# Kernel optimization log

Hardware: AMD Instinct MI355X
Metric: run time of the kernel (lower is better)

The kernel has to match this reference:

```python
import jax, jax.numpy as jnp
import numpy as np

B, S, D_IN, H, D_K = 4, 2048, 512, 8, 64
EPS = 1e-5

def _layer_norm(x, gamma, beta):
    mu = jnp.mean(x, axis=-1, keepdims=True)
    var = jnp.var(x, axis=-1, keepdims=True)
    return (x - mu) * jax.lax.rsqrt(var + EPS) * gamma + beta

def setup_inputs() -> dict:
    key = jax.random.key(0)
    ks = jax.random.split(key, 8)
    d_model = H * D_K
    scale = 1.0 / np.sqrt(D_IN)
    inp = {
        "q": jax.random.normal(ks[0], (B, S, D_IN), jnp.float32),
        "k": jax.random.normal(ks[1], (B, S, D_IN), jnp.float32),
        "v": jax.random.normal(ks[2], (B, S, D_IN), jnp.float32),
        "mask": jnp.ones((B, 1, S, S), jnp.float32),
        "Wq": jax.random.normal(ks[3], (D_IN, d_model), jnp.float32) * scale,
        "bq": jnp.zeros((d_model,), jnp.float32),
        "Wk": jax.random.normal(ks[4], (D_IN, d_model), jnp.float32) * scale,
        "bk": jnp.zeros((d_model,), jnp.float32),
        "Wv": jax.random.normal(ks[5], (D_IN, d_model), jnp.float32) * scale,
        "bv": jnp.zeros((d_model,), jnp.float32),
        "Wo": jax.random.normal(ks[6], (d_model, D_IN), jnp.float32) * (1.0 / np.sqrt(d_model)),
        "bo": jnp.zeros((D_IN,), jnp.float32),
        "gamma": jnp.ones((D_IN,), jnp.float32),
        "beta": jnp.zeros((D_IN,), jnp.float32),
    }
    return inp

def reference(q, k, v, mask, Wq, bq, Wk, bk, Wv, bv, Wo, bo, gamma, beta):
    b, sq, _ = q.shape
    # QKV projections, split heads: [B,S,H*Dk] -> [B,H,S,Dk]
    qh = (q @ Wq + bq).reshape(b, sq, H, D_K).transpose(0, 2, 1, 3)
    kh = (k @ Wk + bk).reshape(b, -1, H, D_K).transpose(0, 2, 1, 3)
    vh = (v @ Wv + bv).reshape(b, -1, H, D_K).transpose(0, 2, 1, 3)
    # scores with multiplicative mask + threshold (non-standard, per source)
    scores = jnp.einsum('bhqd,bhkd->bhqk', qh, kh) / np.sqrt(D_K)
    scores = scores * mask  # mask broadcasts over heads (repeat in torch)
    scores = jnp.where(scores > 0, scores, jnp.float32(-10000.0))
    attn = jax.nn.softmax(scores, axis=-1)
    out = jnp.einsum('bhqk,bhkd->bhqd', attn, vh)
    out = out.transpose(0, 2, 1, 3).reshape(b, sq, H * D_K)
    out = out @ Wo + bo
    return _layer_norm(q + out, gamma, beta)
```

## Files before the change

kernel.cpp:

```cpp
#include <hip/hip_runtime.h>
#include <stdint.h>

typedef __attribute__((ext_vector_type(8))) short s16x8;
typedef __attribute__((ext_vector_type(4))) float f32x4;

__device__ __forceinline__ unsigned short f2bf(float f){
  union { float f; unsigned u; } v; v.f = f;
  return (unsigned short)((v.u + 0x7FFFu + ((v.u>>16)&1u))>>16);
}
__device__ __forceinline__ float bf2f(unsigned short u){
  union { unsigned u; float f; } c; c.u = ((unsigned)u)<<16; return c.f;
}
#if __has_builtin(__builtin_amdgcn_cvt_pk_bf16_f32)
__device__ __forceinline__ unsigned pkbf(float a, float b){
  typedef __attribute__((ext_vector_type(2))) __bf16 bf16x2;
  union { bf16x2 v; unsigned u; } c;
  c.v = __builtin_amdgcn_cvt_pk_bf16_f32(a, b);
  return c.u;
}
#else
__device__ __forceinline__ unsigned pkbf(float a, float b){
  return (unsigned)f2bf(a) | ((unsigned)f2bf(b)<<16);
}
#endif

__device__ __forceinline__ void g2l16(const void* g, void* l){
  auto* lp = reinterpret_cast<__attribute__((address_space(3))) unsigned int*>(
      reinterpret_cast<uintptr_t>(l));
  auto* gp = reinterpret_cast<const __attribute__((address_space(1))) unsigned int*>(
      reinterpret_cast<uintptr_t>(g));
  __builtin_amdgcn_global_load_lds(gp, lp, 16, 0, 0);
}

__global__ __launch_bounds__(256) void cvt_all(
    const float* __restrict__ mask, const float* __restrict__ q,
    const float* __restrict__ k,    const float* __restrict__ v,
    unsigned short* __restrict__ mo, unsigned short* __restrict__ qo,
    unsigned short* __restrict__ ko, unsigned short* __restrict__ vo)
{
  const int z = blockIdx.z;
  const float* src = (z==0)?mask:(z==1)?q:(z==2)?k:v;
  unsigned short* dst = (z==0)?mo:(z==1)?qo:(z==2)?ko:vo;
  const int n = (z==0) ? 4*2048*2048 : 8192*512;
  const int i8 = (blockIdx.x*256 + threadIdx.x)*8;
  if (i8 < n){
    const float4 a = *(const float4*)&src[i8];
    const float4 b = *(const float4*)&src[i8+4];
    uint4 o;
    o.x = pkbf(a.x,a.y); o.y = pkbf(a.z,a.w);
    o.z = pkbf(b.x,b.y); o.w = pkbf(b.z,b.w);
    *(uint4*)&dst[i8] = o;
  }
}

__global__ __launch_bounds__(256) void convert_wT(
    const float* __restrict__ W0, const float* __restrict__ W1,
    const float* __restrict__ W2, const float* __restrict__ W3,
    unsigned short* __restrict__ T0, unsigned short* __restrict__ T1,
    unsigned short* __restrict__ T2, unsigned short* __restrict__ T3)
{
  __shared__ float Ts[64][65];
  const int z = blockIdx.z;
  const float* W = (z==0)?W0:(z==1)?W1:(z==2)?W2:W3;
  unsigned short* Wt = (z==0)?T0:(z==1)?T1:(z==2)?T2:T3;
  const int t = threadIdx.x;
  const int k0 = blockIdx.x*64, n0 = blockIdx.y*64;
  {
    const int r = t>>4, c = (t&15)*4;
#pragma unroll
    for (int rr=0; rr<4; ++rr){
      const float4 w4 = *(const float4*)&W[(size_t)(k0 + r + rr*16)*512 + n0 + c];
      Ts[r+rr*16][c]   = w4.x; Ts[r+rr*16][c+1] = w4.y;
      Ts[r+rr*16][c+2] = w4.z; Ts[r+rr*16][c+3] = w4.w;
    }
  }
  __syncthreads();
  const int n = t>>2, kc = (t&3)*16;
  unsigned o[8];
#pragma unroll
  for (int i=0;i<16;i+=2) o[i>>1] = pkbf(Ts[kc+i][n], Ts[kc+i+1][n]);
  *(uint4*)&Wt[(size_t)(n0+n)*512 + k0 + kc]     = *(uint4*)&o[0];
  *(uint4*)&Wt[(size_t)(n0+n)*512 + k0 + kc + 8] = *(uint4*)&o[4];
}

template<int EPI>
__global__ __launch_bounds__(256) void gemm_m97(
    const unsigned short* __restrict__ A0, const unsigned short* __restrict__ A1,
    const unsigned short* __restrict__ A2,
    const unsigned short* __restrict__ W0, const unsigned short* __restrict__ W1,
    const unsigned short* __restrict__ W2,
    const float* __restrict__ b0, const float* __restrict__ b1, const float* __restrict__ b2,
    unsigned short* __restrict__ Oq, unsigned short* __restrict__ Ok,
    unsigned short* __restrict__ Ov, unsigned short* __restrict__ Oflat)
{
  __shared__ unsigned short As[128*64];
  __shared__ unsigned short Bs[128*64];
  const int t = threadIdx.x;
  const int lane = t & 63;
  const int w = t >> 6;
  const int l16 = lane & 15;
  const int quad = lane >> 4;
  const int wm = w & 1, wn = w >> 1;
  const int bm = blockIdx.x, bn = blockIdx.y;
  const int z = (EPI==0) ? (int)blockIdx.z : 0;
  const unsigned short* A  = (z==0)?A0:(z==1)?A1:A2;
  const unsigned short* Wt = (z==0)?W0:(z==1)?W1:W2;
  const float* bias        = (z==0)?b0:(z==1)?b1:b2;

  const int Lr = lane >> 3;
  const int gc = (lane & 7) ^ Lr;

  f32x4 acc[4][4];
#pragma unroll
  for(int i=0;i<4;i++)
#pragma unroll
    for(int j=0;j<4;j++) acc[i][j] = (f32x4){0.f,0.f,0.f,0.f};

  for (int kt=0; kt<8; ++kt){
    const int k0 = kt*64;
#pragma unroll
    for (int j=0;j<4;++j){
      const int rb = w*32 + j*8;
      g2l16(&A [(size_t)(bm*128 + rb + Lr)*512 + k0 + gc*8], &As[rb*64]);
      g2l16(&Wt[(size_t)(bn*128 + rb + Lr)*512 + k0 + gc*8], &Bs[rb*64]);
    }
    __syncthreads();
#pragma unroll
    for (int kk=0;kk<2;++kk){
      s16x8 af[4], bfr[4];
#pragma unroll
      for (int mt=0;mt<4;++mt){
        const int row = wm*64 + mt*16 + l16;
        af[mt] = *(const s16x8*)&As[row*64 + (((kk*4+quad) ^ (row&7))*8)];
      }
#pragma unroll
      for (int nt=0;nt<4;++nt){
        const int row = wn*64 + nt*16 + l16;
        bfr[nt] = *(const s16x8*)&Bs[row*64 + (((kk*4+quad) ^ (row&7))*8)];
      }
#pragma unroll
      for (int mt=0;mt<4;++mt)
#pragma unroll
        for (int nt=0;nt<4;++nt)
          acc[mt][nt] = __builtin_amdgcn_mfma_f32_16x16x32_bf16(af[mt], bfr[nt], acc[mt][nt], 0,0,0);
    }
    __syncthreads();
  }

#pragma unroll
  for (int mt=0;mt<4;++mt){
    const int gm = bm*128 + wm*64 + mt*16 + quad*4;
    const int b_ = gm>>11, s = gm & 2047;
#pragma unroll
    for (int nt=0;nt<4;++nt){
      const int gn = bn*128 + wn*64 + nt*16 + l16;
      const float bv = bias[gn];
      if (EPI==1){
#pragma unroll
        for (int r=0;r<4;++r)
          Oflat[(size_t)(gm+r)*512 + gn] = f2bf(acc[mt][nt][r] + bv);
      } else if (z==2){
        const int hh = gn>>6, dk = gn&63;
        uint2 uu;
        uu.x = pkbf(acc[mt][nt][0]+bv, acc[mt][nt][1]+bv);
        uu.y = pkbf(acc[mt][nt][2]+bv, acc[mt][nt][3]+bv);
        *(uint2*)&Ov[(((size_t)b_*8 + hh)*64 + dk)*2048 + s] = uu;
      } else {
        const int hh = gn>>6, dk = gn&63;
        unsigned short* Out = (z==0)?Oq:Ok;
        const float scl = (z==0)?0.125f:1.0f;
#pragma unroll
        for (int r=0;r<4;++r)
          Out[(((size_t)b_*8 + hh)*2048 + (s+r))*64 + dk] = f2bf((acc[mt][nt][r]+bv)*scl);
      }
    }
  }
}

__global__ __launch_bounds__(512,4) void attn_kernel(
    const unsigned short* __restrict__ Qp, const unsigned short* __restrict__ Kp,
    const unsigned short* __restrict__ Vt, const unsigned short* __restrict__ maskb,
    unsigned short* __restrict__ Ap)
{
  __shared__ unsigned short Ks[2][64*64];
  __shared__ unsigned short Vs[2][64*64];
  const int t = threadIdx.x;
  const int lane = t & 63;
  const int w = t >> 6;
  const int l16 = lane & 15;
  const int quad = lane >> 4;
  const int h = blockIdx.x, qt = blockIdx.y, b = blockIdx.z;
  const int q0 = qt*128;
  const unsigned short* Qb = Qp + (((size_t)b*8 + h)*2048 + q0)*64;
  const unsigned short* Kb = Kp + ((size_t)b*8 + h)*2048*64;
  const unsigned short* Vb = Vt + ((size_t)b*8 + h)*64*2048;
  const unsigned short* mb = maskb + (size_t)b*2048*2048;

  s16x8 qf[2];
#pragma unroll
  for (int kk=0;kk<2;++kk)
    qf[kk] = *(const s16x8*)&Qb[(size_t)(w*16 + l16)*64 + kk*32 + quad*8];

  const int Lr = lane >> 3;
  const int gc = (lane & 7) ^ Lr;
  const int srow = w*8 + Lr;

  g2l16(&Kb[(size_t)srow*64   + gc*8], &Ks[0][w*8*64]);
  g2l16(&Vb[(size_t)srow*2048 + gc*8], &Vs[0][w*8*64]);

  f32x4 o_acc[4];
#pragma unroll
  for(int nt=0;nt<4;++nt) o_acc[nt]=(f32x4){0.f,0.f,0.f,0.f};
  float l_run = 0.f;

  union U8 { unsigned u[4]; s16x8 v; };
  const int gq = q0 + w*16 + l16;

  for (int kt=0; kt<32; ++kt){
    const int cur = kt&1;
    const int kbase = kt*64;
    __syncthreads();

    uint2 mr[4];
    {
      const unsigned short* mrow = mb + (size_t)gq*2048 + kbase + quad*4;
#pragma unroll
      for (int nt=0;nt<4;++nt) mr[nt] = *(const uint2*)&mrow[nt*16];
    }
    if (kt<31){
      const int kb2 = (kt+1)*64;
      g2l16(&Kb[(size_t)(kb2+srow)*64 + gc*8],   &Ks[cur^1][w*8*64]);
      g2l16(&Vb[(size_t)srow*2048 + kb2 + gc*8], &Vs[cur^1][w*8*64]);
    }

    f32x4 sc[4];
#pragma unroll
    for(int nt=0;nt<4;++nt) sc[nt]=(f32x4){0.f,0.f,0.f,0.f};
#pragma unroll
    for (int nt=0;nt<4;++nt){
      const int row = nt*16 + l16;
      const int rx = row & 7;
      const s16x8 kf0 = *(const s16x8*)&Ks[cur][row*64 + ((quad ^ rx)*8)];
      const s16x8 kf1 = *(const s16x8*)&Ks[cur][row*64 + (((4+quad) ^ rx)*8)];
      sc[nt] = __builtin_amdgcn_mfma_f32_16x16x32_bf16(kf0, qf[0], sc[nt],0,0,0);
      sc[nt] = __builtin_amdgcn_mfma_f32_16x16x32_bf16(kf1, qf[1], sc[nt],0,0,0);
    }
    unsigned pk[8];
    float rs = 0.f;
#pragma unroll
    for (int nt=0;nt<4;++nt){
      const float m0 = bf2f((unsigned short)(mr[nt].x & 0xffffu));
      const float m1 = bf2f((unsigned short)(mr[nt].x >> 16));
      const float m2 = bf2f((unsigned short)(mr[nt].y & 0xffffu));
      const float m3 = bf2f((unsigned short)(mr[nt].y >> 16));
      float x0 = sc[nt][0]*m0, x1 = sc[nt][1]*m1, x2 = sc[nt][2]*m2, x3 = sc[nt][3]*m3;
      x0 = (x0>0.f)?x0:-10000.f; x1 = (x1>0.f)?x1:-10000.f;
      x2 = (x2>0.f)?x2:-10000.f; x3 = (x3>0.f)?x3:-10000.f;
      const float e0 = __expf(x0), e1 = __expf(x1), e2 = __expf(x2), e3 = __expf(x3);
      rs += (e0+e1)+(e2+e3);
      pk[nt*2]   = pkbf(e0, e1);
      pk[nt*2+1] = pkbf(e2, e3);
    }
    rs += __shfl_xor(rs, 16);
    rs += __shfl_xor(rs, 32);
    l_run += rs;
    U8 pu[2];
#pragma unroll
    for (int kk=0;kk<2;++kk)
#pragma unroll
      for (int c=0;c<4;++c){
        const int srcLane = (((quad&1)*2 + (c>>1))<<4) | l16;
        const int vA = __shfl((int)pk[kk*4 + (c&1)],     srcLane);
        const int vB = __shfl((int)pk[kk*4 + 2 + (c&1)], srcLane);
        pu[kk].u[c] = (quad < 2) ? (unsigned)vA : (unsigned)vB;
      }
#pragma unroll
    for (int nt=0;nt<4;++nt){
      const int row = nt*16 + l16;
      const int rx = row & 7;
      const s16x8 vf0 = *(const s16x8*)&Vs[cur][row*64 + ((quad ^ rx)*8)];
      const s16x8 vf1 = *(const s16x8*)&Vs[cur][row*64 + (((4+quad) ^ rx)*8)];
      o_acc[nt] = __builtin_amdgcn_mfma_f32_16x16x32_bf16(vf0, pu[0].v, o_acc[nt],0,0,0);
      o_acc[nt] = __builtin_amdgcn_mfma_f32_16x16x32_bf16(vf1, pu[1].v, o_acc[nt],0,0,0);
    }
  }
  {
    const float inv = 1.0f / l_run;
#pragma unroll
    for (int nt=0;nt<4;++nt){
      uint2 uu;
      uu.x = pkbf(o_acc[nt][0]*inv, o_acc[nt][1]*inv);
      uu.y = pkbf(o_acc[nt][2]*inv, o_acc[nt][3]*inv);
      *(uint2*)&Ap[((size_t)b*2048 + gq)*512 + h*64 + nt*16 + quad*4] = uu;
    }
  }
}

__global__ __launch_bounds__(256) void ln_kernel(
    const float* __restrict__ q, const unsigned short* __restrict__ O2,
    const float* __restrict__ gamma, const float* __restrict__ beta,
    float* __restrict__ out)
{
  const int r = blockIdx.x;
  const int t = threadIdx.x;
  const float* xq = q + (size_t)r * 512;
  const unsigned short* xo = O2 + (size_t)r * 512;
  const float x0 = xq[t]       + bf2f(xo[t]);
  const float x1 = xq[t + 256] + bf2f(xo[t + 256]);
  float s  = x0 + x1;
  float ss = x0*x0 + x1*x1;
#pragma unroll
  for (int off = 1; off < 64; off <<= 1) {
    s  += __shfl_xor(s, off);
    ss += __shfl_xor(ss, off);
  }
  __shared__ float ssum[4], ssq[4];
  const int w = t >> 6;
  if ((t & 63) == 0) { ssum[w] = s; ssq[w] = ss; }
  __syncthreads();
  const float S4 = ssum[0] + ssum[1] + ssum[2] + ssum[3];
  const float Q4 = ssq[0] + ssq[1] + ssq[2] + ssq[3];
  const float mu   = S4 * (1.0f / 512.0f);
  const float var  = Q4 * (1.0f / 512.0f) - mu * mu;
  const float rstd = rsqrtf(var + 1e-5f);
  out[(size_t)r*512 + t]       = (x0 - mu)*rstd*gamma[t] + beta[t];
  out[(size_t)r*512 + t + 256] = (x1 - mu)*rstd*gamma[t+256] + beta[t+256];
}

extern "C" void kernel_launch(void* const* d_in, const int* in_sizes, int n_in,
                              void* d_out, int out_size, void* d_ws, size_t ws_size,
                              hipStream_t stream)
{
  (void)in_sizes; (void)n_in; (void)out_size; (void)ws_size;
  const float* q    = (const float*)d_in[0];
  const float* k    = (const float*)d_in[1];
  const float* v    = (const float*)d_in[2];
  const float* mask = (const float*)d_in[3];
  const float* Wq   = (const float*)d_in[4];
  const float* bq   = (const float*)d_in[5];
  const float* Wk   = (const float*)d_in[6];
  const float* bk   = (const float*)d_in[7];
  const float* Wv   = (const float*)d_in[8];
  const float* bv   = (const float*)d_in[9];
  const float* Wo   = (const float*)d_in[10];
  const float* bo   = (const float*)d_in[11];
  const float* gamma = (const float*)d_in[12];
  const float* beta  = (const float*)d_in[13];
  float* out = (float*)d_out;

  const size_t NT = (size_t)8192*512;
  unsigned short* WtQ  = (unsigned short*)d_ws;
  unsigned short* WtK  = WtQ + 512*512;
  unsigned short* WtV  = WtK + 512*512;
  unsigned short* WtO  = WtV + 512*512;
  unsigned short* Mb   = WtO + 512*512;
  unsigned short* qb   = Mb + (size_t)4*2048*2048;
  unsigned short* kb   = qb + NT;
  unsigned short* vb   = kb + NT;
  unsigned short* Qp   = vb + NT;
  unsigned short* Kp   = Qp + NT;
  unsigned short* Vtg  = Kp + NT;
  unsigned short* Ap   = Vtg + NT;
  unsigned short* O2b  = Ap + NT;

  cvt_all<<<dim3(8192,1,4), 256, 0, stream>>>(mask, q, k, v, Mb, qb, kb, vb);
  convert_wT<<<dim3(8,8,4), 256, 0, stream>>>(Wq, Wk, Wv, Wo, WtQ, WtK, WtV, WtO);
  gemm_m97<0><<<dim3(64,4,3), 256, 0, stream>>>(qb, kb, vb, WtQ, WtK, WtV,
                                                bq, bk, bv, Qp, Kp, Vtg, nullptr);
  attn_kernel<<<dim3(8,16,4), 512, 0, stream>>>(Qp, Kp, Vtg, Mb, Ap);
  gemm_m97<1><<<dim3(64,4,1), 256, 0, stream>>>(Ap, nullptr, nullptr, WtO, nullptr, nullptr,
                                                bo, nullptr, nullptr,
                                                nullptr, nullptr, nullptr, O2b);
  ln_kernel<<<dim3(8192), 256, 0, stream>>>(q, O2b, gamma, beta, out);
}
```

Measured before the change: 311.3 us.

## Merge prep kernels, stage GEMM epilogue via LDS, restructure attention loads

Folds the weight transpose into the input conversion kernel so one launch replaces two. The projection GEMM now writes its Q/K/O outputs through shared memory, giving coalesced 16-byte stores where it previously scattered 2-byte writes. The attention kernel gets a fragment-ordered K layout in LDS and a padded V layout, prefetches the mask one tile ahead in registers, and reorders the grid so heads sit on the y axis. The cost is more registers and LDS per block and a larger prep grid that contains many early-exit blocks.

```diff
diff --git a/kernel.cpp b/kernel.cpp
--- a/kernel.cpp
+++ b/kernel.cpp
@@ -32,55 +32,54 @@
   __builtin_amdgcn_global_load_lds(gp, lp, 16, 0, 0);
 }
 
-__global__ __launch_bounds__(256) void cvt_all(
+__global__ __launch_bounds__(256) void prep_all(
     const float* __restrict__ mask, const float* __restrict__ q,
     const float* __restrict__ k,    const float* __restrict__ v,
+    const float* __restrict__ W0, const float* __restrict__ W1,
+    const float* __restrict__ W2, const float* __restrict__ W3,
     unsigned short* __restrict__ mo, unsigned short* __restrict__ qo,
-    unsigned short* __restrict__ ko, unsigned short* __restrict__ vo)
+    unsigned short* __restrict__ ko, unsigned short* __restrict__ vo,
+    unsigned short* __restrict__ T0, unsigned short* __restrict__ T1,
+    unsigned short* __restrict__ T2, unsigned short* __restrict__ T3)
 {
   const int z = blockIdx.z;
+  const int t = threadIdx.x;
+  if (z == 4){
+    if (blockIdx.x >= 256) return;
+    __shared__ float Ts[64][65];
+    const int wid = blockIdx.x >> 6, within = blockIdx.x & 63;
+    const float* W = (wid==0)?W0:(wid==1)?W1:(wid==2)?W2:W3;
+    unsigned short* Wt = (wid==0)?T0:(wid==1)?T1:(wid==2)?T2:T3;
+    const int k0 = (within>>3)*64, n0 = (within&7)*64;
+    {
+      const int r = t>>4, c = (t&15)*4;
+#pragma unroll
+      for (int rr=0; rr<4; ++rr){
+        const float4 w4 = *(const float4*)&W[(size_t)(k0 + r + rr*16)*512 + n0 + c];
+        Ts[r+rr*16][c]   = w4.x; Ts[r+rr*16][c+1] = w4.y;
+        Ts[r+rr*16][c+2] = w4.z; Ts[r+rr*16][c+3] = w4.w;
+      }
+    }
+    __syncthreads();
+    const int n = t>>2, kc = (t&3)*16;
+    unsigned o[8];
+#pragma unroll
+    for (int i=0;i<16;i+=2) o[i>>1] = pkbf(Ts[kc+i][n], Ts[kc+i+1][n]);
+    *(uint4*)&Wt[(size_t)(n0+n)*512 + k0 + kc]     = *(uint4*)&o[0];
+    *(uint4*)&Wt[(size_t)(n0+n)*512 + k0 + kc + 8] = *(uint4*)&o[4];
+    return;
+  }
   const float* src = (z==0)?mask:(z==1)?q:(z==2)?k:v;
   unsigned short* dst = (z==0)?mo:(z==1)?qo:(z==2)?ko:vo;
-  const int n = (z==0) ? 4*2048*2048 : 8192*512;
-  const int i8 = (blockIdx.x*256 + threadIdx.x)*8;
-  if (i8 < n){
-    const float4 a = *(const float4*)&src[i8];
-    const float4 b = *(const float4*)&src[i8+4];
-    uint4 o;
-    o.x = pkbf(a.x,a.y); o.y = pkbf(a.z,a.w);
-    o.z = pkbf(b.x,b.y); o.w = pkbf(b.z,b.w);
-    *(uint4*)&dst[i8] = o;
-  }
-}
-
-__global__ __launch_bounds__(256) void convert_wT(
-    const float* __restrict__ W0, const float* __restrict__ W1,
-    const float* __restrict__ W2, const float* __restrict__ W3,
-    unsigned short* __restrict__ T0, unsigned short* __restrict__ T1,
-    unsigned short* __restrict__ T2, unsigned short* __restrict__ T3)
-{
-  __shared__ float Ts[64][65];
-  const int z = blockIdx.z;
-  const float* W = (z==0)?W0:(z==1)?W1:(z==2)?W2:W3;
-  unsigned short* Wt = (z==0)?T0:(z==1)?T1:(z==2)?T2:T3;
-  const int t = threadIdx.x;
-  const int k0 = blockIdx.x*64, n0 = blockIdx.y*64;
-  {
-    const int r = t>>4, c = (t&15)*4;
-#pragma unroll
-    for (int rr=0; rr<4; ++rr){
-      const float4 w4 = *(const float4*)&W[(size_t)(k0 + r + rr*16)*512 + n0 + c];
-      Ts[r+rr*16][c]   = w4.x; Ts[r+rr*16][c+1] = w4.y;
-      Ts[r+rr*16][c+2] = w4.z; Ts[r+rr*16][c+3] = w4.w;
-    }
-  }
-  __syncthreads();
-  const int n = t>>2, kc = (t&3)*16;
-  unsigned o[8];
-#pragma unroll
-  for (int i=0;i<16;i+=2) o[i>>1] = pkbf(Ts[kc+i][n], Ts[kc+i+1][n]);
-  *(uint4*)&Wt[(size_t)(n0+n)*512 + k0 + kc]     = *(uint4*)&o[0];
-  *(uint4*)&Wt[(size_t)(n0+n)*512 + k0 + kc + 8] = *(uint4*)&o[4];
+  const int nblk = (z==0) ? 8192 : 2048;
+  if (blockIdx.x >= nblk) return;
+  const size_t i8 = ((size_t)blockIdx.x*256 + t)*8;
+  const float4 a = *(const float4*)&src[i8];
+  const float4 b = *(const float4*)&src[i8+4];
+  uint4 o;
+  o.x = pkbf(a.x,a.y); o.y = pkbf(a.z,a.w);
+  o.z = pkbf(b.x,b.y); o.w = pkbf(b.z,b.w);
+  *(uint4*)&dst[i8] = o;
 }
 
 template<int EPI>
@@ -93,8 +92,9 @@
     unsigned short* __restrict__ Oq, unsigned short* __restrict__ Ok,
     unsigned short* __restrict__ Ov, unsigned short* __restrict__ Oflat)
 {
-  __shared__ unsigned short As[128*64];
-  __shared__ unsigned short Bs[128*64];
+  __shared__ unsigned short SM[2*128*64];
+  unsigned short* As = SM;
+  unsigned short* Bs = SM + 128*64;
   const int t = threadIdx.x;
   const int lane = t & 63;
   const int w = t >> 6;
@@ -147,32 +147,53 @@
     __syncthreads();
   }
 
-#pragma unroll
-  for (int mt=0;mt<4;++mt){
-    const int gm = bm*128 + wm*64 + mt*16 + quad*4;
-    const int b_ = gm>>11, s = gm & 2047;
-#pragma unroll
-    for (int nt=0;nt<4;++nt){
-      const int gn = bn*128 + wn*64 + nt*16 + l16;
-      const float bv = bias[gn];
-      if (EPI==1){
-#pragma unroll
-        for (int r=0;r<4;++r)
-          Oflat[(size_t)(gm+r)*512 + gn] = f2bf(acc[mt][nt][r] + bv);
-      } else if (z==2){
+  if (EPI==0 && z==2){
+#pragma unroll
+    for (int mt=0;mt<4;++mt){
+      const int gm = bm*128 + wm*64 + mt*16 + quad*4;
+      const int b_ = gm>>11, s = gm & 2047;
+#pragma unroll
+      for (int nt=0;nt<4;++nt){
+        const int gn = bn*128 + wn*64 + nt*16 + l16;
+        const float bv = bias[gn];
         const int hh = gn>>6, dk = gn&63;
         uint2 uu;
         uu.x = pkbf(acc[mt][nt][0]+bv, acc[mt][nt][1]+bv);
         uu.y = pkbf(acc[mt][nt][2]+bv, acc[mt][nt][3]+bv);
         *(uint2*)&Ov[(((size_t)b_*8 + hh)*64 + dk)*2048 + s] = uu;
-      } else {
-        const int hh = gn>>6, dk = gn&63;
-        unsigned short* Out = (z==0)?Oq:Ok;
-        const float scl = (z==0)?0.125f:1.0f;
-#pragma unroll
-        for (int r=0;r<4;++r)
-          Out[(((size_t)b_*8 + hh)*2048 + (s+r))*64 + dk] = f2bf((acc[mt][nt][r]+bv)*scl);
-      }
+      }
+    }
+    return;
+  }
+
+  const float scl = (EPI==0 && z==0) ? 0.125f : 1.0f;
+#pragma unroll
+  for (int mt=0;mt<4;++mt){
+    const int rl = wm*64 + mt*16 + quad*4;
+#pragma unroll
+    for (int nt=0;nt<4;++nt){
+      const int cl = wn*64 + nt*16 + l16;
+      const float bv = bias[bn*128 + cl];
+#pragma unroll
+      for (int r=0;r<4;++r)
+        SM[(rl+r)*128 + cl] = f2bf((acc[mt][nt][r] + bv)*scl);
+    }
+  }
+  __syncthreads();
+#pragma unroll
+  for (int i=0;i<8;++i){
+    const int u = t*8 + i;
+    const int row = u >> 4, seg = u & 15;
+    const uint4 val = *(const uint4*)&SM[row*128 + seg*8];
+    if (EPI==1){
+      *(uint4*)&Oflat[(size_t)(bm*128+row)*512 + bn*128 + seg*8] = val;
+    } else {
+      const int col = bn*128 + seg*8;
+      const int hh = col>>6, dk = col&63;
+      const int gm2 = bm*128 + row;
+      const int b_ = gm2>>11, s = gm2&2047;
+      unsigned short* Out = (z==0)?Oq:Ok;
+      *(uint4*)&Out[(((size_t)b_*8 + hh)*2048 + s)*64 + dk] = val;
     }
   }
 }
@@ -182,77 +203,75 @@
     const unsigned short* __restrict__ Vt, const unsigned short* __restrict__ maskb,
     unsigned short* __restrict__ Ap)
 {
-  __shared__ unsigned short Ks[2][64*64];
-  __shared__ unsigned short Vs[2][64*64];
+  __shared__ unsigned short Ks[2][8*512];
+  __shared__ unsigned short Vs[2][8*528];
   const int t = threadIdx.x;
   const int lane = t & 63;
   const int w = t >> 6;
   const int l16 = lane & 15;
   const int quad = lane >> 4;
-  const int h = blockIdx.x, qt = blockIdx.y, b = blockIdx.z;
-  const int q0 = qt*128;
-  const unsigned short* Qb = Qp + (((size_t)b*8 + h)*2048 + q0)*64;
+  const int g = blockIdx.x;
+  const int h = blockIdx.y;
+  const int qt = g & 15, b = g >> 4;
+  const int q0 = qt*128 + w*16;
+  const unsigned short* Qb = Qp + ((size_t)b*8 + h)*2048*64;
   const unsigned short* Kb = Kp + ((size_t)b*8 + h)*2048*64;
   const unsigned short* Vb = Vt + ((size_t)b*8 + h)*64*2048;
-  const unsigned short* mb = maskb + (size_t)b*2048*2048;
+  const unsigned short* mb = maskb + (size_t)b*2048*2048 + (size_t)(q0 + l16)*2048 + quad*4;
 
   s16x8 qf[2];
 #pragma unroll
   for (int kk=0;kk<2;++kk)
-    qf[kk] = *(const s16x8*)&Qb[(size_t)(w*16 + l16)*64 + kk*32 + quad*8];
-
-  const int Lr = lane >> 3;
-  const int gc = (lane & 7) ^ Lr;
-  const int srow = w*8 + Lr;
-
-  g2l16(&Kb[(size_t)srow*64   + gc*8], &Ks[0][w*8*64]);
-  g2l16(&Vb[(size_t)srow*2048 + gc*8], &Vs[0][w*8*64]);
+    qf[kk] = *(const s16x8*)&Qb[(size_t)(q0 + l16)*64 + kk*32 + quad*8];
+
+  const int koff = (((w>>1)*16 + l16)*64) + (((w&1)*4 + quad)*8);
+  const int voff = ((w*8 + (lane>>3))*2048) + (((lane&7) ^ (lane>>3))*8);
+
+  g2l16(Kb + koff, &Ks[0][w*512]);
+  g2l16(Vb + voff, &Vs[0][w*528]);
+  uint2 mcur[4], mnext[4];
+#pragma unroll
+  for (int nt=0;nt<4;++nt) mcur[nt] = *(const uint2*)&mb[nt*16];
 
   f32x4 o_acc[4];
 #pragma unroll
   for(int nt=0;nt<4;++nt) o_acc[nt]=(f32x4){0.f,0.f,0.f,0.f};
   float l_run = 0.f;
 
+  const int b3 = l16>>3, a7 = l16&7;
   union U8 { unsigned u[4]; s16x8 v; };
-  const int gq = q0 + w*16 + l16;
 
   for (int kt=0; kt<32; ++kt){
     const int cur = kt&1;
-    const int kbase = kt*64;
     __syncthreads();
 
-    uint2 mr[4];
-    {
-      const unsigned short* mrow = mb + (size_t)gq*2048 + kbase + quad*4;
-#pragma unroll
-      for (int nt=0;nt<4;++nt) mr[nt] = *(const uint2*)&mrow[nt*16];
-    }
     if (kt<31){
       const int kb2 = (kt+1)*64;
-      g2l16(&Kb[(size_t)(kb2+srow)*64 + gc*8],   &Ks[cur^1][w*8*64]);
-      g2l16(&Vb[(size_t)srow*2048 + kb2 + gc*8], &Vs[cur^1][w*8*64]);
+      g2l16(Kb + (size_t)kb2*64 + koff, &Ks[cur^1][w*512]);
+      g2l16(Vb + kb2 + voff,            &Vs[cur^1][w*528]);
+#pragma unroll
+      for (int nt=0;nt<4;++nt) mnext[nt] = *(const uint2*)&mb[kb2 + nt*16];
     }
 
     f32x4 sc[4];
 #pragma unroll
     for(int nt=0;nt<4;++nt) sc[nt]=(f32x4){0.f,0.f,0.f,0.f};
 #pragma unroll
-    for (int nt=0;nt<4;++nt){
-      const int row = nt*16 + l16;
-      const int rx = row & 7;
-      const s16x8 kf0 = *(const s16x8*)&Ks[cur][row*64 + ((quad ^ rx)*8)];
-      const s16x8 kf1 = *(const s16x8*)&Ks[cur][row*64 + (((4+quad) ^ rx)*8)];
-      sc[nt] = __builtin_amdgcn_mfma_f32_16x16x32_bf16(kf0, qf[0], sc[nt],0,0,0);
-      sc[nt] = __builtin_amdgcn_mfma_f32_16x16x32_bf16(kf1, qf[1], sc[nt],0,0,0);
-    }
+    for (int nt=0;nt<4;++nt)
+#pragma unroll
+      for (int kk=0;kk<2;++kk){
+        const s16x8 kf = *(const s16x8*)&Ks[cur][(nt*2+kk)*512 + lane*8];
+        sc[nt] = __builtin_amdgcn_mfma_f32_16x16x32_bf16(kf, qf[kk], sc[nt],0,0,0);
+      }
+
     unsigned pk[8];
     float rs = 0.f;
 #pragma unroll
     for (int nt=0;nt<4;++nt){
-      const float m0 = bf2f((unsigned short)(mr[nt].x & 0xffffu));
-      const float m1 = bf2f((unsigned short)(mr[nt].x >> 16));
-      const float m2 = bf2f((unsigned short)(mr[nt].y & 0xffffu));
-      const float m3 = bf2f((unsigned short)(mr[nt].y >> 16));
+      const float m0 = bf2f((unsigned short)(mcur[nt].x & 0xffffu));
+      const float m1 = bf2f((unsigned short)(mcur[nt].x >> 16));
+      const float m2 = bf2f((unsigned short)(mcur[nt].y & 0xffffu));
+      const float m3 = bf2f((unsigned short)(mcur[nt].y >> 16));
       float x0 = sc[nt][0]*m0, x1 = sc[nt][1]*m1, x2 = sc[nt][2]*m2, x3 = sc[nt][3]*m3;
       x0 = (x0>0.f)?x0:-10000.f; x1 = (x1>0.f)?x1:-10000.f;
       x2 = (x2>0.f)?x2:-10000.f; x3 = (x3>0.f)?x3:-10000.f;
@@ -275,23 +294,26 @@
         pu[kk].u[c] = (quad < 2) ? (unsigned)vA : (unsigned)vB;
       }
 #pragma unroll
-    for (int nt=0;nt<4;++nt){
-      const int row = nt*16 + l16;
-      const int rx = row & 7;
-      const s16x8 vf0 = *(const s16x8*)&Vs[cur][row*64 + ((quad ^ rx)*8)];
-      const s16x8 vf1 = *(const s16x8*)&Vs[cur][row*64 + (((4+quad) ^ rx)*8)];
-      o_acc[nt] = __builtin_amdgcn_mfma_f32_16x16x32_bf16(vf0, pu[0].v, o_acc[nt],0,0,0);
-      o_acc[nt] = __builtin_amdgcn_mfma_f32_16x16x32_bf16(vf1, pu[1].v, o_acc[nt],0,0,0);
-    }
-  }
+    for (int ot=0;ot<4;++ot){
+#pragma unroll
+      for (int kk=0;kk<2;++kk){
+        const s16x8 vf = *(const s16x8*)&Vs[cur][(ot*2+b3)*528 + a7*64 + (((kk*4+quad)^a7)*8)];
+        o_acc[ot] = __builtin_amdgcn_mfma_f32_16x16x32_bf16(vf, pu[kk].v, o_acc[ot],0,0,0);
+      }
+    }
+#pragma unroll
+    for (int nt=0;nt<4;++nt) mcur[nt] = mnext[nt];
+  }
+
   {
     const float inv = 1.0f / l_run;
-#pragma unroll
-    for (int nt=0;nt<4;++nt){
+    const int gq = q0 + l16;
+#pragma unroll
+    for (int ot=0;ot<4;++ot){
       uint2 uu;
-      uu.x = pkbf(o_acc[nt][0]*inv, o_acc[nt][1]*inv);
-      uu.y = pkbf(o_acc[nt][2]*inv, o_acc[nt][3]*inv);
-      *(uint2*)&Ap[((size_t)b*2048 + gq)*512 + h*64 + nt*16 + quad*4] = uu;
+      uu.x = pkbf(o_acc[ot][0]*inv, o_acc[ot][1]*inv);
+      uu.y = pkbf(o_acc[ot][2]*inv, o_acc[ot][3]*inv);
+      *(uint2*)&Ap[((size_t)b*2048 + gq)*512 + h*64 + ot*16 + quad*4] = uu;
     }
   }
 }
@@ -363,11 +385,11 @@
   unsigned short* Ap   = Vtg + NT;
   unsigned short* O2b  = Ap + NT;
 
-  cvt_all<<<dim3(8192,1,4), 256, 0, stream>>>(mask, q, k, v, Mb, qb, kb, vb);
-  convert_wT<<<dim3(8,8,4), 256, 0, stream>>>(Wq, Wk, Wv, Wo, WtQ, WtK, WtV, WtO);
+  prep_all<<<dim3(8192,1,5), 256, 0, stream>>>(mask, q, k, v, Wq, Wk, Wv, Wo,
+                                               Mb, qb, kb, vb, WtQ, WtK, WtV, WtO);
   gemm_m97<0><<<dim3(64,4,3), 256, 0, stream>>>(qb, kb, vb, WtQ, WtK, WtV,
                                                 bq, bk, bv, Qp, Kp, Vtg, nullptr);
-  attn_kernel<<<dim3(8,16,4), 512, 0, stream>>>(Qp, Kp, Vtg, Mb, Ap);
+  attn_kernel<<<dim3(64,8), 512, 0, stream>>>(Qp, Kp, Vtg, Mb, Ap);
   gemm_m97<1><<<dim3(64,4,1), 256, 0, stream>>>(Ap, nullptr, nullptr, WtO, nullptr, nullptr,
                                                 bo, nullptr, nullptr,
                                                 nullptr, nullptr, nullptr, O2b);
```

Result: faster. 305.1 us (-2.0%).
